# Optimization experiments

Measured on AMD Instinct MI355X. Metric: run time of the kernel, lower is better.

## Reference

```python
import jax, jax.numpy as jnp
import numpy as np

IN_CH = 384
OUT_CH = 384
EPS = 1e-5  # torch LayerNorm default


def setup_inputs() -> dict:
    key = jax.random.key(0)
    k1, k2, k3 = jax.random.split(key, 3)
    x = jax.random.normal(k1, (32, IN_CH, 64, 64), dtype=jnp.float32)
    # LayerNorm params (torch defaults: gamma=1, beta=0; randomize slightly for a stronger test)
    ln_weight = jnp.ones((IN_CH,), jnp.float32) + 0.01 * jax.random.normal(k2, (IN_CH,), jnp.float32)
    ln_bias = jnp.zeros((IN_CH,), jnp.float32)
    # Linear params, kaiming-uniform-ish scale
    bound = 1.0 / np.sqrt(IN_CH)
    W = jax.random.uniform(k3, (OUT_CH, IN_CH), jnp.float32, -bound, bound)
    b = jnp.zeros((OUT_CH,), jnp.float32)
    return {"x": x, "ln_weight": ln_weight, "ln_bias": ln_bias, "W": W, "b": b}


def reference(x, ln_weight, ln_bias, W, b):
    # x: [B, C, H, W] -> normalize over channel dim, project C->OUT_CH, GELU, back to NCHW
    xh = jnp.transpose(x, (0, 2, 3, 1))  # [B, H, W, C]
    mu = jnp.mean(xh, axis=-1, keepdims=True)
    var = jnp.mean(jnp.square(xh - mu), axis=-1, keepdims=True)
    xn = (xh - mu) * jax.lax.rsqrt(var + EPS) * ln_weight + ln_bias
    y = jnp.einsum('bhwc,oc->bhwo', xn, W) + b
    y = jax.nn.gelu(y, approximate=False)  # torch nn.GELU default is exact erf form
    return jnp.transpose(y, (0, 3, 1, 2))  # [B, OUT_CH, H, W]
```

## Files before the change

kernel.cpp:

```cpp
#include <hip/hip_runtime.h>
#include <hip/hip_bf16.h>
#include <cmath>

typedef float f32x4 __attribute__((ext_vector_type(4)));
typedef float f32x16 __attribute__((ext_vector_type(16)));
typedef __bf16 bf16x4 __attribute__((ext_vector_type(4)));
typedef __bf16 bf16x8 __attribute__((ext_vector_type(8)));

#define C_IN 384
#define C_OUT 384
#define SPB 4096
#define NPIX 131072
#define BP 64
#define LDK 392

__global__ __launch_bounds__(128) void ppl_prep_kernel(const float* __restrict__ W,
                                                       const float* __restrict__ gamma,
                                                       const float* __restrict__ beta,
                                                       const float* __restrict__ bias,
                                                       __bf16* __restrict__ Wp,
                                                       float* __restrict__ t1,
                                                       float* __restrict__ t2) {
  const int o = blockIdx.x;
  const int t = threadIdx.x;
  const float* row = W + o * C_IN;
  float s1 = 0.f, s2 = 0.f;
  for (int c = t; c < C_IN; c += 128) {
    const float w = row[c];
    const __bf16 wq = (__bf16)(w * gamma[c]);
    Wp[o * C_IN + c] = wq;
    s1 += (float)wq;
    s2 += beta[c] * w;
  }
#pragma unroll
  for (int off = 32; off > 0; off >>= 1) {
    s1 += __shfl_down(s1, off);
    s2 += __shfl_down(s2, off);
  }
  __shared__ float red[2][2];
  if ((t & 63) == 0) { red[t >> 6][0] = s1; red[t >> 6][1] = s2; }
  __syncthreads();
  if (t == 0) {
    t1[o] = red[0][0] + red[1][0];
    t2[o] = red[0][1] + red[1][1] + bias[o];
  }
}

__device__ __forceinline__ float gelu_fast(float v) {
  const float u = 0.7978845608028654f * v * __builtin_fmaf(0.044715f * v, v, 1.0f);
  const float e = __expf(-2.0f * u);
  return v * __builtin_amdgcn_rcpf(1.0f + e);
}

__global__ __launch_bounds__(256, 3) void ppl_fused_kernel(const float* __restrict__ x,
                                                           const __bf16* __restrict__ Wp,
                                                           const float* __restrict__ t1g,
                                                           const float* __restrict__ t2g,
                                                           float* __restrict__ out) {
  __shared__ __bf16 Xs[BP][LDK];
  __shared__ float sS[4][BP];
  __shared__ float sQ[4][BP];
  __shared__ float mu_s[BP];
  __shared__ float rs_s[BP];

  const int tid = threadIdx.x;
  const int w = tid >> 6;
  const int lane = tid & 63;
  const int q = tid & 15;
  const int j = tid >> 4;
  const int col = lane & 31;
  const int hi = lane >> 5;
  const int p0 = blockIdx.x * BP;
  const int b = p0 >> 12;
  const int s0 = p0 & 4095;
  const int ob = w * 96;

  const float* xq = x + (size_t)b * (C_IN * SPB) + s0 + 4 * q;

  f32x4 LA[12], LB[12];
#pragma unroll
  for (int i = 0; i < 3; ++i)
#pragma unroll
    for (int m = 0; m < 4; ++m)
      LA[i * 4 + m] = *reinterpret_cast<const f32x4*>(xq + (size_t)(64 * i + 4 * j + m) * SPB);
#pragma unroll
  for (int i = 0; i < 3; ++i)
#pragma unroll
    for (int m = 0; m < 4; ++m)
      LB[i * 4 + m] = *reinterpret_cast<const f32x4*>(xq + (size_t)(64 * (i + 3) + 4 * j + m) * SPB);

  float ss[4] = {0.f, 0.f, 0.f, 0.f};
  float qq[4] = {0.f, 0.f, 0.f, 0.f};

#define PROCESS(L, ibase)                                                   \
  {                                                                         \
    _Pragma("unroll") for (int i = 0; i < 3; ++i) {                         \
      _Pragma("unroll") for (int r = 0; r < 4; ++r) {                       \
        const float f0 = L[i * 4 + 0][r];                                   \
        const float f1 = L[i * 4 + 1][r];                                   \
        const float f2 = L[i * 4 + 2][r];                                   \
        const float f3 = L[i * 4 + 3][r];                                   \
        ss[r] += (f0 + f1) + (f2 + f3);                                     \
        qq[r] += (f0 * f0 + f1 * f1) + (f2 * f2 + f3 * f3);                 \
        bf16x4 pk;                                                          \
        pk[0] = (__bf16)f0; pk[1] = (__bf16)f1;                             \
        pk[2] = (__bf16)f2; pk[3] = (__bf16)f3;                             \
        *reinterpret_cast<bf16x4*>(&Xs[4 * q + r][64 * ((ibase) + i) + 4 * j]) = pk; \
      }                                                                     \
    }                                                                       \
  }

  PROCESS(LA, 0)
  PROCESS(LB, 3)
#undef PROCESS

#pragma unroll
  for (int r = 0; r < 4; ++r) {
    ss[r] += __shfl_xor(ss[r], 16);
    ss[r] += __shfl_xor(ss[r], 32);
    qq[r] += __shfl_xor(qq[r], 16);
    qq[r] += __shfl_xor(qq[r], 32);
  }
  if (lane < 16) {
#pragma unroll
    for (int r = 0; r < 4; ++r) {
      sS[w][4 * lane + r] = ss[r];
      sQ[w][4 * lane + r] = qq[r];
    }
  }
  __syncthreads();
  if (tid < BP) {
    const float st = sS[0][tid] + sS[1][tid] + sS[2][tid] + sS[3][tid];
    const float qt = sQ[0][tid] + sQ[1][tid] + sQ[2][tid] + sQ[3][tid];
    const float m = st * (1.0f / C_IN);
    mu_s[tid] = m;
    rs_s[tid] = rsqrtf(qt * (1.0f / C_IN) - m * m + 1e-5f);
  }
  __syncthreads();

  const __bf16* wp0 = Wp + (size_t)(ob + col) * C_IN + hi * 8;
  const __bf16* wp1 = wp0 + 32 * C_IN;
  const __bf16* wp2 = wp0 + 64 * C_IN;
  const __bf16* xs0 = &Xs[col][hi * 8];
  const __bf16* xs1 = &Xs[32 + col][hi * 8];

  f32x16 acc[2][3];
#pragma unroll
  for (int m = 0; m < 2; ++m)
#pragma unroll
    for (int n = 0; n < 3; ++n)
#pragma unroll
      for (int r = 0; r < 16; ++r) acc[m][n][r] = 0.f;

#define LOADB(dst, kk)                                     \
  {                                                        \
    dst[0] = *reinterpret_cast<const bf16x8*>(wp0 + (kk)); \
    dst[1] = *reinterpret_cast<const bf16x8*>(wp1 + (kk)); \
    dst[2] = *reinterpret_cast<const bf16x8*>(wp2 + (kk)); \
  }
#define STEP(bb, kk)                                                                    \
  {                                                                                     \
    const bf16x8 a0 = *reinterpret_cast<const bf16x8*>(xs0 + (kk));                     \
    const bf16x8 a1 = *reinterpret_cast<const bf16x8*>(xs1 + (kk));                     \
    acc[0][0] = __builtin_amdgcn_mfma_f32_32x32x16_bf16(a0, bb[0], acc[0][0], 0, 0, 0); \
    acc[0][1] = __builtin_amdgcn_mfma_f32_32x32x16_bf16(a0, bb[1], acc[0][1], 0, 0, 0); \
    acc[0][2] = __builtin_amdgcn_mfma_f32_32x32x16_bf16(a0, bb[2], acc[0][2], 0, 0, 0); \
    acc[1][0] = __builtin_amdgcn_mfma_f32_32x32x16_bf16(a1, bb[0], acc[1][0], 0, 0, 0); \
    acc[1][1] = __builtin_amdgcn_mfma_f32_32x32x16_bf16(a1, bb[1], acc[1][1], 0, 0, 0); \
    acc[1][2] = __builtin_amdgcn_mfma_f32_32x32x16_bf16(a1, bb[2], acc[1][2], 0, 0, 0); \
  }

  {
    bf16x8 bA[3], bB[3];
    LOADB(bA, 0);
#pragma unroll
    for (int it = 0; it < 12; ++it) {
      const int k = it * 32;
      LOADB(bB, k + 16);
      STEP(bA, k);
      if (it < 11) LOADB(bA, k + 32);
      STEP(bB, k + 16);
    }
  }
#undef LOADB
#undef STEP

  const float t1v[3] = {t1g[ob + col], t1g[ob + 32 + col], t1g[ob + 64 + col]};
  const float t2v[3] = {t2g[ob + col], t2g[ob + 32 + col], t2g[ob + 64 + col]};
  float* outp = out + (((size_t)(b * C_OUT + ob + col)) << 12) + s0;

#pragma unroll
  for (int nf = 0; nf < 3; ++nf) {
    float* op = outp + ((size_t)nf << 17);
#pragma unroll
    for (int m = 0; m < 2; ++m) {
#pragma unroll
      for (int qd = 0; qd < 4; ++qd) {
        const int pr = m * 32 + qd * 8 + hi * 4;
        const f32x4 mu4 = *reinterpret_cast<const f32x4*>(&mu_s[pr]);
        const f32x4 rs4 = *reinterpret_cast<const f32x4*>(&rs_s[pr]);
        f32x4 y;
#pragma unroll
        for (int r = 0; r < 4; ++r) {
          const float val = rs4[r] * (acc[m][nf][qd * 4 + r] - mu4[r] * t1v[nf]) + t2v[nf];
          y[r] = gelu_fast(val);
        }
        *reinterpret_cast<f32x4*>(op + pr) = y;
      }
    }
  }
}

extern "C" void kernel_launch(void* const* d_in, const int* in_sizes, int n_in,
                              void* d_out, int out_size, void* d_ws, size_t ws_size,
                              hipStream_t stream) {
  const float* x = (const float*)d_in[0];
  const float* gamma = (const float*)d_in[1];
  const float* beta = (const float*)d_in[2];
  const float* W = (const float*)d_in[3];
  const float* bias = (const float*)d_in[4];
  float* out = (float*)d_out;

  __bf16* Wp = (__bf16*)d_ws;
  float* t1 = (float*)(Wp + C_OUT * C_IN);
  float* t2 = t1 + C_OUT;

  ppl_prep_kernel<<<C_OUT, 128, 0, stream>>>(W, gamma, beta, bias, Wp, t1, t2);
  ppl_fused_kernel<<<NPIX / BP, 256, 0, stream>>>(x, Wp, t1, t2, out);
}
```

Before: 176.5 us.

## Split fused LayerNorm-GEMM into stats/cast pass and bf16 GEMM pass

Adds a pre-pass kernel that computes per-pixel mean and rstd and writes a bf16 copy of x, followed by a GEMM kernel that loads the bf16 tile and the precomputed stats. This is meant to decouple the strided fp32 load and reduction from the MFMA kernel and so lower its register and latency pressure. It costs an extra round trip of a bf16 copy of the activations through memory. The new path is taken only when the workspace is large enough, otherwise it falls back to the fused kernel.

Result: slower. 183.8 us (+4.2%).

```diff
diff --git a/kernel.cpp b/kernel.cpp
--- a/kernel.cpp
+++ b/kernel.cpp
@@ -4,6 +4,7 @@
 
 typedef float f32x4 __attribute__((ext_vector_type(4)));
 typedef float f32x16 __attribute__((ext_vector_type(16)));
+typedef __bf16 bf16x2 __attribute__((ext_vector_type(2)));
 typedef __bf16 bf16x4 __attribute__((ext_vector_type(4)));
 typedef __bf16 bf16x8 __attribute__((ext_vector_type(8)));
 
@@ -52,6 +53,176 @@
   return v * __builtin_amdgcn_rcpf(1.0f + e);
 }
 
+__global__ __launch_bounds__(512) void ppl_stats_cast_kernel(const float* __restrict__ x,
+                                                             __bf16* __restrict__ xb,
+                                                             float* __restrict__ mu,
+                                                             float* __restrict__ rs) {
+  __shared__ float sS[8][256];
+  __shared__ float sQ[8][256];
+  const int tid = threadIdx.x;
+  const int w = tid >> 6;
+  const int lane = tid & 63;
+  const int p0 = blockIdx.x * 256;
+  const int b = p0 >> 12;
+  const int s0 = p0 & 4095;
+  const int c0 = w * 48;
+  const float* xp = x + (((size_t)(b * C_IN + c0)) << 12) + s0 + 4 * lane;
+  __bf16* xbp = xb + (((size_t)(b * C_IN + c0)) << 12) + s0 + 4 * lane;
+
+  f32x4 ssv = {0.f, 0.f, 0.f, 0.f};
+  f32x4 qqv = {0.f, 0.f, 0.f, 0.f};
+#pragma unroll
+  for (int i = 0; i < 48; i += 12) {
+    f32x4 L[12];
+#pragma unroll
+    for (int j = 0; j < 12; ++j)
+      L[j] = *reinterpret_cast<const f32x4*>(xp + ((size_t)(i + j) << 12));
+#pragma unroll
+    for (int j = 0; j < 12; ++j) {
+      const f32x4 v = L[j];
+      ssv += v;
+      qqv += v * v;
+      bf16x4 pk;
+      pk[0] = (__bf16)v[0];
+      pk[1] = (__bf16)v[1];
+      pk[2] = (__bf16)v[2];
+      pk[3] = (__bf16)v[3];
+      *reinterpret_cast<bf16x4*>(xbp + ((size_t)(i + j) << 12)) = pk;
+    }
+  }
+  *reinterpret_cast<f32x4*>(&sS[w][4 * lane]) = ssv;
+  *reinterpret_cast<f32x4*>(&sQ[w][4 * lane]) = qqv;
+  __syncthreads();
+  if (tid < 256) {
+    float st = 0.f, qt = 0.f;
+#pragma unroll
+    for (int r = 0; r < 8; ++r) {
+      st += sS[r][tid];
+      qt += sQ[r][tid];
+    }
+    const float m = st * (1.0f / C_IN);
+    mu[p0 + tid] = m;
+    rs[p0 + tid] = rsqrtf(qt * (1.0f / C_IN) - m * m + 1e-5f);
+  }
+}
+
+__global__ __launch_bounds__(256, 3) void ppl_gemm2_kernel(const __bf16* __restrict__ xb,
+                                                           const __bf16* __restrict__ Wp,
+                                                           const float* __restrict__ mug,
+                                                           const float* __restrict__ rsg,
+                                                           const float* __restrict__ t1g,
+                                                           const float* __restrict__ t2g,
+                                                           float* __restrict__ out) {
+  __shared__ __bf16 Xs[BP][LDK];
+  __shared__ float mu_s[BP];
+  __shared__ float rs_s[BP];
+
+  const int tid = threadIdx.x;
+  const int w = tid >> 6;
+  const int lane = tid & 63;
+  const int col = lane & 31;
+  const int hi = lane >> 5;
+  const int p0 = blockIdx.x * BP;
+  const int b = p0 >> 12;
+  const int s0 = p0 & 4095;
+  const int ob = w * 96;
+
+  if (tid < BP) {
+    mu_s[tid] = mug[p0 + tid];
+    rs_s[tid] = rsg[p0 + tid];
+  }
+
+  const int chg = tid >> 3;
+  const int px8 = (tid & 7) * 8;
+  const __bf16* xsrc = xb + (((size_t)(b * C_IN)) << 12) + s0 + px8;
+#pragma unroll
+  for (int i = 0; i < 6; ++i) {
+    const int c = 2 * chg + 64 * i;
+    const bf16x8 v0 = *reinterpret_cast<const bf16x8*>(xsrc + ((size_t)c << 12));
+    const bf16x8 v1 = *reinterpret_cast<const bf16x8*>(xsrc + ((size_t)(c + 1) << 12));
+#pragma unroll
+    for (int r = 0; r < 8; ++r) {
+      bf16x2 pr;
+      pr[0] = v0[r];
+      pr[1] = v1[r];
+      *reinterpret_cast<bf16x2*>(&Xs[px8 + r][c]) = pr;
+    }
+  }
+  __syncthreads();
+
+  const __bf16* wp0 = Wp + (size_t)(ob + col) * C_IN + hi * 8;
+  const __bf16* wp1 = wp0 + 32 * C_IN;
+  const __bf16* wp2 = wp0 + 64 * C_IN;
+  const __bf16* xs0 = &Xs[col][hi * 8];
+  const __bf16* xs1 = &Xs[32 + col][hi * 8];
+
+  f32x16 acc[2][3];
+#pragma unroll
+  for (int m = 0; m < 2; ++m)
+#pragma unroll
+    for (int n = 0; n < 3; ++n)
+#pragma unroll
+      for (int r = 0; r < 16; ++r) acc[m][n][r] = 0.f;
+
+#define LOADB(dst, kk)                                     \
+  {                                                        \
+    dst[0] = *reinterpret_cast<const bf16x8*>(wp0 + (kk)); \
+    dst[1] = *reinterpret_cast<const bf16x8*>(wp1 + (kk)); \
+    dst[2] = *reinterpret_cast<const bf16x8*>(wp2 + (kk)); \
+  }
+#define STEP(bb, kk)                                                                    \
+  {                                                                                     \
+    const bf16x8 a0 = *reinterpret_cast<const bf16x8*>(xs0 + (kk));                     \
+    const bf16x8 a1 = *reinterpret_cast<const bf16x8*>(xs1 + (kk));                     \
+    acc[0][0] = __builtin_amdgcn_mfma_f32_32x32x16_bf16(a0, bb[0], acc[0][0], 0, 0, 0); \
+    acc[0][1] = __builtin_amdgcn_mfma_f32_32x32x16_bf16(a0, bb[1], acc[0][1], 0, 0, 0); \
+    acc[0][2] = __builtin_amdgcn_mfma_f32_32x32x16_bf16(a0, bb[2], acc[0][2], 0, 0, 0); \
+    acc[1][0] = __builtin_amdgcn_mfma_f32_32x32x16_bf16(a1, bb[0], acc[1][0], 0, 0, 0); \
+    acc[1][1] = __builtin_amdgcn_mfma_f32_32x32x16_bf16(a1, bb[1], acc[1][1], 0, 0, 0); \
+    acc[1][2] = __builtin_amdgcn_mfma_f32_32x32x16_bf16(a1, bb[2], acc[1][2], 0, 0, 0); \
+  }
+
+  {
+    bf16x8 bA[3], bB[3];
+    LOADB(bA, 0);
+#pragma unroll
+    for (int it = 0; it < 12; ++it) {
+      const int k = it * 32;
+      LOADB(bB, k + 16);
+      STEP(bA, k);
+      if (it < 11) LOADB(bA, k + 32);
+      STEP(bB, k + 16);
+    }
+  }
+#undef LOADB
+#undef STEP
+
+  const float t1v[3] = {t1g[ob + col], t1g[ob + 32 + col], t1g[ob + 64 + col]};
+  const float t2v[3] = {t2g[ob + col], t2g[ob + 32 + col], t2g[ob + 64 + col]};
+  float* outp = out + (((size_t)(b * C_OUT + ob + col)) << 12) + s0;
+
+#pragma unroll
+  for (int nf = 0; nf < 3; ++nf) {
+    float* op = outp + ((size_t)nf << 17);
+#pragma unroll
+    for (int m = 0; m < 2; ++m) {
+#pragma unroll
+      for (int qd = 0; qd < 4; ++qd) {
+        const int pr = m * 32 + qd * 8 + hi * 4;
+        const f32x4 mu4 = *reinterpret_cast<const f32x4*>(&mu_s[pr]);
+        const f32x4 rs4 = *reinterpret_cast<const f32x4*>(&rs_s[pr]);
+        f32x4 y;
+#pragma unroll
+        for (int r = 0; r < 4; ++r) {
+          const float val = rs4[r] * (acc[m][nf][qd * 4 + r] - mu4[r] * t1v[nf]) + t2v[nf];
+          y[r] = gelu_fast(val);
+        }
+        *reinterpret_cast<f32x4*>(op + pr) = y;
+      }
+    }
+  }
+}
+
 __global__ __launch_bounds__(256, 3) void ppl_fused_kernel(const float* __restrict__ x,
                                                            const __bf16* __restrict__ Wp,
                                                            const float* __restrict__ t1g,
@@ -109,7 +280,6 @@
       }                                                                     \
     }                                                                       \
   }
-
   PROCESS(LA, 0)
   PROCESS(LB, 3)
 #undef PROCESS
@@ -169,7 +339,6 @@
     acc[1][1] = __builtin_amdgcn_mfma_f32_32x32x16_bf16(a1, bb[1], acc[1][1], 0, 0, 0); \
     acc[1][2] = __builtin_amdgcn_mfma_f32_32x32x16_bf16(a1, bb[2], acc[1][2], 0, 0, 0); \
   }
-
   {
     bf16x8 bA[3], bB[3];
     LOADB(bA, 0);
@@ -188,7 +357,6 @@
   const float t1v[3] = {t1g[ob + col], t1g[ob + 32 + col], t1g[ob + 64 + col]};
   const float t2v[3] = {t2g[ob + col], t2g[ob + 32 + col], t2g[ob + 64 + col]};
   float* outp = out + (((size_t)(b * C_OUT + ob + col)) << 12) + s0;
-
 #pragma unroll
   for (int nf = 0; nf < 3; ++nf) {
     float* op = outp + ((size_t)nf << 17);
@@ -224,7 +392,19 @@
   __bf16* Wp = (__bf16*)d_ws;
   float* t1 = (float*)(Wp + C_OUT * C_IN);
   float* t2 = t1 + C_OUT;
+  float* mu = t2 + C_OUT;
+  float* rs = mu + NPIX;
+  __bf16* xb = (__bf16*)(rs + NPIX);
+
+  const size_t need = (size_t)C_OUT * C_IN * 2 + 2 * C_OUT * 4 +
+                      2 * (size_t)NPIX * 4 + (size_t)NPIX * C_IN * 2;
 
   ppl_prep_kernel<<<C_OUT, 128, 0, stream>>>(W, gamma, beta, bias, Wp, t1, t2);
-  ppl_fused_kernel<<<NPIX / BP, 256, 0, stream>>>(x, Wp, t1, t2, out);
-}
+
+  if (ws_size >= need) {
+    ppl_stats_cast_kernel<<<NPIX / 256, 512, 0, stream>>>(x, xb, mu, rs);
+    ppl_gemm2_kernel<<<NPIX / BP, 256, 0, stream>>>(xb, Wp, mu, rs, t1, t2, out);
+  } else {
+    ppl_fused_kernel<<<NPIX / BP, 256, 0, stream>>>(x, Wp, t1, t2, out);
+  }
+}
```
